# Kernel tuning notes

Measured on AMD Instinct MI355X. Metric: run time of the kernel, lower is better.

Reference implementation:

```python
import jax, jax.numpy as jnp
import numpy as np

B, N, E = 64, 512, 8192          # graphs, nodes per graph, edges per graph
F_IN, H, C = 128, 128, 10        # in features, hidden, classes
K1, K2 = 256, 128                # dense pool cluster counts: ceil(.5*N), ceil(.5*K1)
EPS = 1e-15


def setup_inputs():
    key = jax.random.key(0)
    keys = jax.random.split(key, 32)
    it = iter(keys)
    def w(shape, fan_in):
        return jax.random.normal(next(it), shape, jnp.float32) / np.sqrt(fan_in)
    x = jax.random.normal(next(it), (B * N, F_IN), jnp.float32)
    src_l = jax.random.randint(next(it), (B, E), 0, N)
    dst_l = jax.random.randint(next(it), (B, E), 0, N)
    off = (jnp.arange(B) * N)[:, None]
    src = (src_l + off).reshape(-1).astype(jnp.int32)
    dst = (dst_l + off).reshape(-1).astype(jnp.int32)
    return dict(
        x=x, src=src, dst=dst,
        conv0_wr=w((F_IN, H), F_IN), conv0_wroot=w((F_IN, H), F_IN), conv0_b=jnp.zeros((H,), jnp.float32),
        sconv2_wr=w((H, H), H), sconv2_wroot=w((H, H), H), sconv2_b=jnp.zeros((H,), jnp.float32),
        sconv3_wr=w((H, H), H), sconv3_wroot=w((H, H), H), sconv3_b=jnp.zeros((H,), jnp.float32),
        sage1_wr=w((H, H), H), sage1_wroot=w((H, H), H), sage1_b=jnp.zeros((H,), jnp.float32),
        sage2_wr=w((H, H), H), sage2_wroot=w((H, H), H), sage2_b=jnp.zeros((H,), jnp.float32),
        pool0_w=w((H, K1), H), pool0_b=jnp.zeros((K1,), jnp.float32),
        pool1_w=w((H, K2), H), pool1_b=jnp.zeros((K2,), jnp.float32),
        p1=w((H,), H), p2=w((H,), H), p3=w((H,), H),
        lin1_1_w=w((2 * H, H), 2 * H), lin1_1_b=jnp.zeros((H,), jnp.float32),
        lin1_w=w((H, H), H), lin1_b=jnp.zeros((H,), jnp.float32),
        lin2_w=w((2 * H, C), 2 * H), lin2_b=jnp.zeros((C,), jnp.float32),
    )


def _graph_conv(x, src, dst, emask, wr, wroot, b, n):
    # PyG GraphConv: lin_rel(sum_j x_j) + lin_root(x_i); invalid edges masked to 0.
    msg = x[src] * emask[:, None]
    agg = jax.ops.segment_sum(msg, dst, num_segments=n)
    return agg @ wr + x @ wroot + b


def _topk_pool(x, score_w, src, dst, emask, n_per_graph, k):
    # TopK pooling (MPoolS): score = x.w/||w||, keep top ratio*n per graph, gate by tanh(score).
    score = x @ score_w / (jnp.linalg.norm(score_w) + 1e-16)
    idx = jax.lax.top_k(score.reshape(B, n_per_graph), k)[1]
    perm = (idx + (jnp.arange(B) * n_per_graph)[:, None]).reshape(-1)
    new_x = x[perm] * jnp.tanh(score[perm])[:, None]
    new_id = jnp.full((B * n_per_graph,), -1, jnp.int32).at[perm].set(
        jnp.arange(B * k, dtype=jnp.int32))
    ns, nd = new_id[src], new_id[dst]
    valid = (ns >= 0) & (nd >= 0) & (emask > 0)
    return new_x, jnp.where(valid, ns, 0), jnp.where(valid, nd, 0), valid.astype(x.dtype)


def _readout(x, k):
    # gmp || gap per graph (nodes are contiguous, k per graph)
    xr = x.reshape(B, k, -1)
    return jnp.concatenate([xr.max(axis=1), xr.mean(axis=1)], axis=-1)


def _dense_sage(x, adj, wr, wroot, b):
    agg = (adj @ x) / jnp.clip(adj.sum(-1, keepdims=True), 1.0, None)
    return agg @ wr + x @ wroot + b


def _dense_mincut_pool(x, adj, s):
    s = jax.nn.softmax(s, axis=-1)
    k = s.shape[-1]
    out = jnp.einsum('bnk,bnf->bkf', s, x)
    out_adj = jnp.einsum('bnk,bnm,bml->bkl', s, adj, s)
    mincut_num = jnp.trace(out_adj, axis1=-2, axis2=-1)
    deg = adj.sum(-1)
    mincut_den = jnp.einsum('bn,bnk,bnk->b', deg, s, s)
    mc = -jnp.mean(mincut_num / (mincut_den + EPS))
    ss = jnp.einsum('bnk,bnl->bkl', s, s)
    ss_n = jnp.linalg.norm(ss, axis=(1, 2), keepdims=True)
    eye = jnp.eye(k, dtype=x.dtype)
    o = jnp.mean(jnp.linalg.norm(ss / (ss_n + EPS) - eye / jnp.sqrt(k), axis=(1, 2)))
    di = jnp.arange(k)
    out_adj = out_adj.at[:, di, di].set(0.0)
    dpool = jnp.sqrt(out_adj.sum(-1)) + EPS
    out_adj = out_adj / dpool[:, :, None] / dpool[:, None, :]
    return out, out_adj, mc, o


def _forward(x, src, dst, conv0_wr, conv0_wroot, conv0_b, sconv2_wr, sconv2_wroot, sconv2_b,
             sconv3_wr, sconv3_wroot, sconv3_b, sage1_wr, sage1_wroot, sage1_b,
             sage2_wr, sage2_wroot, sage2_b, pool0_w, pool0_b, pool1_w, pool1_b,
             p1, p2, p3, lin1_1_w, lin1_1_b, lin1_w, lin1_b, lin2_w, lin2_b):
    relu = jax.nn.relu
    e0 = jnp.ones((src.shape[0],), x.dtype)
    x0 = relu(_graph_conv(x, src, dst, e0, conv0_wr, conv0_wroot, conv0_b, B * N))
    # ---- sparse (MPoolS / top-k) branch, stage 1 ----
    sx, s1, d1, m1 = _topk_pool(x0, p1, src, dst, e0, N, N // 2)
    sx1 = _readout(sx, N // 2)
    # ---- dense (DiffPool-style) branch ----
    xd = x0.reshape(B, N, H)                               # to_dense_batch (full mask)
    g = src // N
    adj = jnp.zeros((B, N, N), x.dtype).at[g, src % N, dst % N].add(1.0)  # to_dense_adj
    s = xd @ pool0_w + pool0_b
    xd, adj, mc, o = _dense_mincut_pool(xd, adj, s)
    xd = relu(_dense_sage(xd, adj, sage1_wr, sage1_wroot, sage1_b))
    s = xd @ pool1_w + pool1_b
    xd, adj, mc2, o2 = _dense_mincut_pool(xd, adj, s)
    mc, o = mc + mc2, o + o2
    xd = _dense_sage(xd, adj, sage2_wr, sage2_wroot, sage2_b)
    xg = relu(xd.mean(axis=1) @ lin1_w + lin1_b)
    # ---- sparse branch, stages 2 and 3 ----
    sx = relu(_graph_conv(sx, s1, d1, m1, sconv2_wr, sconv2_wroot, sconv2_b, B * (N // 2)))
    sx, s2, d2, m2 = _topk_pool(sx, p2, s1, d1, m1, N // 2, N // 4)
    sx2 = _readout(sx, N // 4)
    sx = relu(_graph_conv(sx, s2, d2, m2, sconv3_wr, sconv3_wroot, sconv3_b, B * (N // 4)))
    sx, s3, d3, m3 = _topk_pool(sx, p3, s2, d2, m2, N // 4, N // 8)
    sx3 = _readout(sx, N // 8)
    sxr = relu((sx1 + sx2 + sx3) @ lin1_1_w + lin1_1_b)
    logits = jnp.concatenate([sxr, xg], axis=-1) @ lin2_w + lin2_b
    return logits, mc, o


def reference(x, src, dst, conv0_wr, conv0_wroot, conv0_b, sconv2_wr, sconv2_wroot, sconv2_b,
              sconv3_wr, sconv3_wroot, sconv3_b, sage1_wr, sage1_wroot, sage1_b,
              sage2_wr, sage2_wroot, sage2_b, pool0_w, pool0_b, pool1_w, pool1_b,
              p1, p2, p3, lin1_1_w, lin1_1_b, lin1_w, lin1_b, lin2_w, lin2_b):
    return _forward(x, src, dst, conv0_wr, conv0_wroot, conv0_b, sconv2_wr, sconv2_wroot,
                    sconv2_b, sconv3_wr, sconv3_wroot, sconv3_b, sage1_wr, sage1_wroot,
                    sage1_b, sage2_wr, sage2_wroot, sage2_b, pool0_w, pool0_b, pool1_w,
                    pool1_b, p1, p2, p3, lin1_1_w, lin1_1_b, lin1_w, lin1_b, lin2_w, lin2_b)
```

## Files before the change

kernel.cpp:

```cpp
#include <hip/hip_runtime.h>
#include <math.h>

#define NGRAPH 64
#define NE 524288
#define EPG 8192
#define TSZ 2560

typedef short s16x8 __attribute__((ext_vector_type(8)));
typedef float f32x4 __attribute__((ext_vector_type(4)));

__device__ inline unsigned short f2bf(float f) {
    unsigned int u = __float_as_uint(f);
    return (unsigned short)((u + 0x7FFFu + ((u >> 16) & 1u)) >> 16);
}

__global__ void edge_count2(const int* __restrict__ keyA, int* __restrict__ cntA,
                            const int* __restrict__ keyB, int* __restrict__ cntB) {
    int e = blockIdx.x * 256 + threadIdx.x;
    if (e >= NE) return;
    if (blockIdx.y == 0) atomicAdd(&cntA[keyA[e]], 1);
    else                 atomicAdd(&cntB[keyB[e]], 1);
}

__device__ inline void scan_body(const int* __restrict__ counts, int* __restrict__ offs,
                                 int* __restrict__ cursor, int nPerGraph,
                                 float* __restrict__ degOut, int* s) {
    const int g = blockIdx.x, t = threadIdx.x;
    int v = (t < nPerGraph) ? counts[g * nPerGraph + t] : 0;
    s[t] = v; __syncthreads();
    for (int d = 1; d < 512; d <<= 1) {
        int u = (t >= d) ? s[t - d] : 0;
        __syncthreads();
        s[t] += u;
        __syncthreads();
    }
    if (t < nPerGraph) {
        int o = g * EPG + s[t] - v;
        offs[g * nPerGraph + t] = o;
        cursor[g * nPerGraph + t] = o;
        if (degOut) degOut[g * nPerGraph + t] = (float)v;
    }
}

__global__ __launch_bounds__(512) void scan_offsets(const int* __restrict__ counts,
        int* __restrict__ offs, int* __restrict__ cursor, int nPerGraph,
        float* __restrict__ degOut) {
    __shared__ int s[512];
    scan_body(counts, offs, cursor, nPerGraph, degOut, s);
}

__global__ __launch_bounds__(512) void scan_offsets2(
        const int* __restrict__ cA, int* __restrict__ oA, int* __restrict__ uA,
        const int* __restrict__ cB, int* __restrict__ oB, int* __restrict__ uB,
        int nPerGraph, float* __restrict__ degB) {
    __shared__ int s[512];
    if (blockIdx.y == 0) scan_body(cA, oA, uA, nPerGraph, nullptr, s);
    else                 scan_body(cB, oB, uB, nPerGraph, degB, s);
}

__global__ void edge_fill(const int* __restrict__ key, const int* __restrict__ payload,
                          const float* __restrict__ mask, int* __restrict__ cursor,
                          int* __restrict__ elist) {
    int e = blockIdx.x * 256 + threadIdx.x;
    if (e < NE && (!mask || mask[e] > 0.f)) {
        int p = atomicAdd(&cursor[key[e]], 1);
        elist[p] = payload[e];
    }
}

__global__ void edge_fill2(const int* __restrict__ kA, const int* __restrict__ pA,
                           int* __restrict__ uA, int* __restrict__ eA,
                           const int* __restrict__ kB, const int* __restrict__ pB,
                           int* __restrict__ uB, int* __restrict__ eB) {
    int e = blockIdx.x * 256 + threadIdx.x;
    if (e >= NE) return;
    if (blockIdx.y == 0) { int p = atomicAdd(&uA[kA[e]], 1); eA[p] = pA[e]; }
    else                 { int p = atomicAdd(&uB[kB[e]], 1); eB[p] = pB[e]; }
}

__global__ __launch_bounds__(256) void gather_csr(
    const float* __restrict__ xfeat, int Fx,
    const int* __restrict__ offs, const int* __restrict__ cnts,
    const int* __restrict__ elist,
    float* __restrict__ out, int totRows, int rowsPerGraph)
{
    const int gid = (blockIdx.x * 256 + threadIdx.x) >> 5;
    const int lane = threadIdx.x & 31;
    const int csh = (Fx == 256) ? 1 : 0;
    const int rid = gid >> csh;
    const int c0 = (gid & ((1 << csh) - 1)) << 7;
    if (rid >= totRows) return;
    const int row = (rid & 63) * rowsPerGraph + (rid >> 6);
    const int beg = offs[row];
    const int n = cnts[row];
    const long long co = (long long)c0 + (lane << 2);
    float4 acc = make_float4(0.f, 0.f, 0.f, 0.f);
    int j = 0;
    for (; j + 4 <= n; j += 4) {
        const int n0 = elist[beg + j], n1 = elist[beg + j + 1];
        const int n2 = elist[beg + j + 2], n3 = elist[beg + j + 3];
        const float4 v0 = *(const float4*)&xfeat[(long long)n0 * Fx + co];
        const float4 v1 = *(const float4*)&xfeat[(long long)n1 * Fx + co];
        const float4 v2 = *(const float4*)&xfeat[(long long)n2 * Fx + co];
        const float4 v3 = *(const float4*)&xfeat[(long long)n3 * Fx + co];
        acc.x += v0.x + v1.x + v2.x + v3.x;
        acc.y += v0.y + v1.y + v2.y + v3.y;
        acc.z += v0.z + v1.z + v2.z + v3.z;
        acc.w += v0.w + v1.w + v2.w + v3.w;
    }
    for (; j < n; ++j) {
        const float4 v = *(const float4*)&xfeat[(long long)elist[beg + j] * Fx + co];
        acc.x += v.x; acc.y += v.y; acc.z += v.z; acc.w += v.w;
    }
    *(float4*)&out[(long long)row * Fx + co] = acc;
}

struct WSpec {
    const float* w1; const float* w2; int K1; int K2; int Nn;
    unsigned short* oh; unsigned short* ol;
};

__global__ void wconv_all(WSpec s0, WSpec s1, WSpec s2, WSpec s3, WSpec s4, WSpec s5, WSpec s6) {
    WSpec s;
    switch (blockIdx.y) {
        case 0: s = s0; break; case 1: s = s1; break; case 2: s = s2; break;
        case 3: s = s3; break; case 4: s = s4; break; case 5: s = s5; break;
        default: s = s6; break;
    }
    int idx = blockIdx.x * 256 + threadIdx.x;
    int Kt = s.K1 + s.K2;
    if (idx >= s.Nn * Kt) return;
    int n = idx / Kt, k = idx - n * Kt;
    float v = (k < s.K1) ? s.w1[(long long)k * s.Nn + n] : s.w2[(long long)(k - s.K1) * s.Nn + n];
    unsigned short h = f2bf(v);
    s.oh[idx] = h;
    s.ol[idx] = f2bf(v - __uint_as_float((unsigned int)h << 16));
}

__device__ inline void stageN_split(const float* __restrict__ src, int ldk, int k0,
                                    short* lds, int tid, const float* __restrict__ rs, int m0) {
    const int r = tid >> 2, kq = (tid & 3) << 3;
    const float* p = src + (long long)r * ldk + k0 + kq;
    float v[8];
    *(float4*)v = *(const float4*)p;
    *(float4*)(v + 4) = *(const float4*)(p + 4);
    if (rs) { float s = rs[m0 + r]; for (int i = 0; i < 8; ++i) v[i] *= s; }
    s16x8 hv, lv;
    #pragma unroll
    for (int i = 0; i < 8; ++i) {
        unsigned short h = f2bf(v[i]);
        float hf = __uint_as_float((unsigned int)h << 16);
        hv[i] = (short)h;
        lv[i] = (short)f2bf(v[i] - hf);
    }
    *(s16x8*)(lds + r * 40 + kq) = hv;
    *(s16x8*)(lds + TSZ + r * 40 + kq) = lv;
}

__device__ inline void stageT_split(const float* __restrict__ src, int ldm, int k0, int m0,
                                    short* lds, int tid) {
    const int kp = tid >> 4, mc = tid & 15;
    const int k = kp << 1;
    const float* p0 = src + (long long)(k0 + k) * ldm + m0 + mc;
    const float* p1 = p0 + ldm;
    #pragma unroll
    for (int i = 0; i < 4; ++i) {
        float a = p0[i << 4], b = p1[i << 4];
        unsigned short ha = f2bf(a), hb = f2bf(b);
        float hfa = __uint_as_float((unsigned int)ha << 16);
        float hfb = __uint_as_float((unsigned int)hb << 16);
        unsigned short la = f2bf(a - hfa), lb = f2bf(b - hfb);
        const int o = (mc + (i << 4)) * 40 + k;
        *(unsigned int*)(lds + o) = (unsigned int)ha | ((unsigned int)hb << 16);
        *(unsigned int*)(lds + o + TSZ) = (unsigned int)la | ((unsigned int)lb << 16);
    }
}

__device__ inline void stageT_hi(const float* __restrict__ src, int ldm, int k0, int m0,
                                 short* lds, int tid) {
    const int kp = tid >> 4, mc = tid & 15;
    const int k = kp << 1;
    const float* p0 = src + (long long)(k0 + k) * ldm + m0 + mc;
    const float* p1 = p0 + ldm;
    #pragma unroll
    for (int i = 0; i < 4; ++i) {
        unsigned short ha = f2bf(p0[i << 4]), hb = f2bf(p1[i << 4]);
        *(unsigned int*)(lds + (mc + (i << 4)) * 40 + k) =
            (unsigned int)ha | ((unsigned int)hb << 16);
    }
}

__device__ inline void stageW_split(const unsigned short* __restrict__ wh,
                                    const unsigned short* __restrict__ wl, int ldk,
                                    int n0, int k0, short* lds, int tid) {
    const int r = tid >> 2, kq = (tid & 3) << 3;
    *(s16x8*)(lds + r * 40 + kq) = *(const s16x8*)(wh + (long long)(n0 + r) * ldk + k0 + kq);
    *(s16x8*)(lds + TSZ + r * 40 + kq) = *(const s16x8*)(wl + (long long)(n0 + r) * ldk + k0 + kq);
}

__device__ inline void mfma_split(const short* As, const short* Bs, int wm, int wn,
                                  int l15, int quad, f32x4 (&acc)[2][2]) {
    const int ko = quad << 3;
    s16x8 ah[2], al[2], bh[2], bl[2];
    #pragma unroll
    for (int i = 0; i < 2; ++i) {
        const int ra = (wm + (i << 4) + l15) * 40 + ko;
        const int rb = (wn + (i << 4) + l15) * 40 + ko;
        ah[i] = *(const s16x8*)&As[ra];
        al[i] = *(const s16x8*)&As[TSZ + ra];
        bh[i] = *(const s16x8*)&Bs[rb];
        bl[i] = *(const s16x8*)&Bs[TSZ + rb];
    }
    #pragma unroll
    for (int mi = 0; mi < 2; ++mi)
    #pragma unroll
    for (int ni = 0; ni < 2; ++ni) {
        f32x4 c = acc[mi][ni];
        c = __builtin_amdgcn_mfma_f32_16x16x32_bf16(ah[mi], bh[ni], c, 0, 0, 0);
        c = __builtin_amdgcn_mfma_f32_16x16x32_bf16(ah[mi], bl[ni], c, 0, 0, 0);
        c = __builtin_amdgcn_mfma_f32_16x16x32_bf16(al[mi], bh[ni], c, 0, 0, 0);
        acc[mi][ni] = c;
    }
}

__device__ inline void mfma_hi(const short* As, const short* Bs, int wm, int wn,
                               int l15, int quad, f32x4 (&acc)[2][2]) {
    const int ko = quad << 3;
    s16x8 ah[2], bh[2];
    #pragma unroll
    for (int i = 0; i < 2; ++i) {
        ah[i] = *(const s16x8*)&As[(wm + (i << 4) + l15) * 40 + ko];
        bh[i] = *(const s16x8*)&Bs[(wn + (i << 4) + l15) * 40 + ko];
    }
    #pragma unroll
    for (int mi = 0; mi < 2; ++mi)
    #pragma unroll
    for (int ni = 0; ni < 2; ++ni)
        acc[mi][ni] = __builtin_amdgcn_mfma_f32_16x16x32_bf16(ah[mi], bh[ni], acc[mi][ni], 0, 0, 0);
}

__global__ __launch_bounds__(256) void gemm_aw(
    const float* __restrict__ A1, int K1, const float* __restrict__ A2, int K2,
    const float* __restrict__ rscale,
    const unsigned short* __restrict__ Wh, const unsigned short* __restrict__ Wl,
    const float* __restrict__ bias, float* __restrict__ C, int Nn, int doRelu)
{
    __shared__ short As[2 * TSZ], Bs[2 * TSZ];
    const int m0 = blockIdx.y << 6, n0 = blockIdx.x << 6;
    const int tid = threadIdx.x, lane = tid & 63, wv = tid >> 6;
    const int l15 = lane & 15, quad = lane >> 4;
    const int wm = (wv & 1) << 5, wn = (wv >> 1) << 5;
    f32x4 acc[2][2] = {};
    const int Kt = K1 + K2;
    for (int k0 = 0; k0 < Kt; k0 += 32) {
        if (k0 < K1) stageN_split(A1 + (long long)m0 * K1, K1, k0, As, tid, rscale, m0);
        else         stageN_split(A2 + (long long)m0 * K2, K2, k0 - K1, As, tid, nullptr, 0);
        stageW_split(Wh, Wl, Kt, n0, k0, Bs, tid);
        __syncthreads();
        mfma_split(As, Bs, wm, wn, l15, quad, acc);
        __syncthreads();
    }
    #pragma unroll
    for (int mi = 0; mi < 2; ++mi)
    #pragma unroll
    for (int ni = 0; ni < 2; ++ni) {
        const int col = n0 + wn + (ni << 4) + l15;
        const float bv = bias ? bias[col] : 0.f;
        #pragma unroll
        for (int r = 0; r < 4; ++r) {
            const int row = m0 + wm + (mi << 4) + (quad << 2) + r;
            float v = acc[mi][ni][r] + bv;
            if (doRelu) v = fmaxf(v, 0.f);
            C[(long long)row * Nn + col] = v;
        }
    }
}

__global__ __launch_bounds__(256) void gemm_tt(
    const float* __restrict__ At, const float* __restrict__ Bkn,
    float* __restrict__ C, float* __restrict__ fro,
    int Kd, int Mm, int Nn, int dual,
    long long sA, long long sB, long long sC)
{
    __shared__ short As[2 * TSZ], Bs[2 * TSZ], A2s[TSZ];
    __shared__ float redf[4];
    const int z = blockIdx.x;
    const float* Ap = At + (long long)z * sA;
    const float* Bp = Bkn + (long long)z * sB;
    const int m0 = blockIdx.y << 6, n0 = blockIdx.z << 6;
    const int tid = threadIdx.x, lane = tid & 63, wv = tid >> 6;
    const int l15 = lane & 15, quad = lane >> 4;
    const int wm = (wv & 1) << 5, wn = (wv >> 1) << 5;
    const int fw = dual ? ((m0 < n0) ? 2 : ((m0 == n0) ? 1 : 0)) : 0;
    f32x4 acc[2][2] = {};
    f32x4 accA[2][2] = {};
    for (int k0 = 0; k0 < Kd; k0 += 32) {
        stageT_split(Ap, Mm, k0, m0, As, tid);
        stageT_split(Bp, Nn, k0, n0, Bs, tid);
        if (fw) stageT_hi(Ap, Mm, k0, n0, A2s, tid);
        __syncthreads();
        mfma_split(As, Bs, wm, wn, l15, quad, acc);
        if (fw) mfma_hi(As, A2s, wm, wn, l15, quad, accA);
        __syncthreads();
    }
    float* Cp = C + (long long)z * sC;
    #pragma unroll
    for (int mi = 0; mi < 2; ++mi)
    #pragma unroll
    for (int ni = 0; ni < 2; ++ni) {
        const int col = n0 + wn + (ni << 4) + l15;
        #pragma unroll
        for (int r = 0; r < 4; ++r) {
            const int row = m0 + wm + (mi << 4) + (quad << 2) + r;
            Cp[(long long)row * Nn + col] = acc[mi][ni][r];
        }
    }
    if (fw) {
        float s = 0.f;
        #pragma unroll
        for (int mi = 0; mi < 2; ++mi)
        #pragma unroll
        for (int ni = 0; ni < 2; ++ni)
        #pragma unroll
        for (int r = 0; r < 4; ++r) s += accA[mi][ni][r] * accA[mi][ni][r];
        s *= (float)fw;
        for (int off = 32; off; off >>= 1) s += __shfl_xor(s, off);
        if (lane == 0) redf[wv] = s;
        __syncthreads();
        if (tid == 0) atomicAdd(&fro[z], redf[0] + redf[1] + redf[2] + redf[3]);
    }
}

__global__ __launch_bounds__(256) void gemm_nt(
    const float* __restrict__ A, const float* __restrict__ Bkn, float* __restrict__ C,
    int Kd, int Nn, long long sA, long long sB, long long sC)
{
    __shared__ short As[2 * TSZ], Bs[2 * TSZ];
    const int z = blockIdx.x;
    const int m0 = blockIdx.y << 6, n0 = blockIdx.z << 6;
    const float* Ap = A + (long long)z * sA + (long long)m0 * Kd;
    const float* Bp = Bkn + (long long)z * sB;
    const int tid = threadIdx.x, lane = tid & 63, wv = tid >> 6;
    const int l15 = lane & 15, quad = lane >> 4;
    const int wm = (wv & 1) << 5, wn = (wv >> 1) << 5;
    f32x4 acc[2][2] = {};
    for (int k0 = 0; k0 < Kd; k0 += 32) {
        stageN_split(Ap, Kd, k0, As, tid, nullptr, 0);
        stageT_split(Bp, Nn, k0, n0, Bs, tid);
        __syncthreads();
        mfma_split(As, Bs, wm, wn, l15, quad, acc);
        __syncthreads();
    }
    float* Cp = C + (long long)z * sC;
    #pragma unroll
    for (int mi = 0; mi < 2; ++mi)
    #pragma unroll
    for (int ni = 0; ni < 2; ++ni) {
        const int col = n0 + wn + (ni << 4) + l15;
        #pragma unroll
        for (int r = 0; r < 4; ++r) {
            const int row = m0 + wm + (mi << 4) + (quad << 2) + r;
            Cp[(long long)row * Nn + col] = acc[mi][ni][r];
        }
    }
}

__global__ __launch_bounds__(256) void softmax_rows_wave(
    float* __restrict__ sm, int L,
    const float* __restrict__ deg,
    float* __restrict__ rowq2, float* __restrict__ rowdq2, int totRows)
{
    const int wid = (blockIdx.x * 256 + threadIdx.x) >> 6;
    const int lane = threadIdx.x & 63;
    if (wid >= totRows) return;
    float* rowp = sm + (long long)wid * L;
    const int nv = L >> 6;
    float v[4];
    if (nv == 4) {
        float4 t = *(const float4*)&rowp[lane << 2];
        v[0] = t.x; v[1] = t.y; v[2] = t.z; v[3] = t.w;
    } else {
        float2 t = *(const float2*)&rowp[lane << 1];
        v[0] = t.x; v[1] = t.y;
    }
    float mx = v[0];
    for (int i = 1; i < nv; ++i) mx = fmaxf(mx, v[i]);
    for (int off = 32; off; off >>= 1) mx = fmaxf(mx, __shfl_xor(mx, off));
    float s = 0.f;
    for (int i = 0; i < nv; ++i) { v[i] = expf(v[i] - mx); s += v[i]; }
    for (int off = 32; off; off >>= 1) s += __shfl_xor(s, off);
    const float inv = 1.f / s;
    float q2 = 0.f;
    for (int i = 0; i < nv; ++i) { float p = v[i] * inv; v[i] = p; q2 += p * p; }
    if (nv == 4) *(float4*)&rowp[lane << 2] = make_float4(v[0], v[1], v[2], v[3]);
    else         *(float2*)&rowp[lane << 1] = make_float2(v[0], v[1]);
    for (int off = 32; off; off >>= 1) q2 += __shfl_xor(q2, off);
    if (lane == 0) { rowq2[wid] = q2; rowdq2[wid] = deg[wid] * q2; }
}

__global__ __launch_bounds__(256) void zdiag_rowsum_wave(
    float* __restrict__ adj, int K, float* __restrict__ dpool,
    float* __restrict__ rowdiag, int totRows)
{
    const int wid = (blockIdx.x * 256 + threadIdx.x) >> 6;
    const int lane = threadIdx.x & 63;
    if (wid >= totRows) return;
    const int b = wid / K;
    const int dcol = wid - b * K;
    float* rowp = adj + (long long)wid * K;
    const int nv = K >> 6;
    float s = 0.f, dval = 0.f;
    for (int q = 0; q < nv; ++q) {
        int c = lane + (q << 6);
        float v = rowp[c];
        if (c == dcol) { dval = v; rowp[c] = 0.f; v = 0.f; }
        s += v;
    }
    for (int off = 32; off; off >>= 1) s += __shfl_xor(s, off);
    if (lane == (dcol & 63)) rowdiag[wid] = dval;
    if (lane == 0) dpool[wid] = sqrtf(s) + 1e-15f;
}

__global__ __launch_bounds__(256) void norm_adj_wave(
    float* __restrict__ adj, int K, const float* __restrict__ dpool,
    float* __restrict__ rowsum, float* __restrict__ rscale, int totRows)
{
    const int wid = (blockIdx.x * 256 + threadIdx.x) >> 6;
    const int lane = threadIdx.x & 63;
    if (wid >= totRows) return;
    const int b = wid / K;
    float* rowp = adj + (long long)wid * K;
    const float inv_r = 1.f / dpool[wid];
    const int nv = K >> 6;
    float s = 0.f;
    for (int q = 0; q < nv; ++q) {
        int c = lane + (q << 6);
        float v = rowp[c] * inv_r / dpool[b * K + c];
        rowp[c] = v;
        s += v;
    }
    for (int off = 32; off; off >>= 1) s += __shfl_xor(s, off);
    if (lane == 0) { rowsum[wid] = s; rscale[wid] = 1.f / fmaxf(s, 1.f); }
}

__global__ __launch_bounds__(256) void reduce2_pergraph(
    const float* __restrict__ a, const float* __restrict__ b, int rowsPerGraph,
    float* __restrict__ outA, float* __restrict__ outB)
{
    __shared__ float redA[4], redB[4];
    const int g = blockIdx.x, t = threadIdx.x;
    float sa = 0.f, sb = 0.f;
    for (int i = t; i < rowsPerGraph; i += 256) {
        sa += a[g * rowsPerGraph + i];
        if (b) sb += b[g * rowsPerGraph + i];
    }
    for (int off = 32; off; off >>= 1) { sa += __shfl_xor(sa, off); sb += __shfl_xor(sb, off); }
    const int wv = t >> 6;
    if ((t & 63) == 0) { redA[wv] = sa; redB[wv] = sb; }
    __syncthreads();
    if (t == 0) {
        outA[g] = redA[0] + redA[1] + redA[2] + redA[3];
        if (outB) outB[g] = redB[0] + redB[1] + redB[2] + redB[3];
    }
}

__global__ __launch_bounds__(512) void topk_kernel(
    const float* __restrict__ x, const float* __restrict__ p, int n, int k,
    int* __restrict__ new_id, int* __restrict__ sel, float* __restrict__ gate)
{
    __shared__ float sc[512];
    __shared__ int pref[512];
    const int g = blockIdx.x, tid = threadIdx.x;
    float myScore = 0.f;
    if (tid < n) {
        const float* xr = x + (long long)(g * n + tid) * 128;
        float pn2 = 0.f, d = 0.f;
        #pragma unroll 4
        for (int f = 0; f < 128; f += 4) {
            float4 pv = *(const float4*)&p[f];
            float4 v = *(const float4*)&xr[f];
            pn2 += pv.x * pv.x + pv.y * pv.y + pv.z * pv.z + pv.w * pv.w;
            d += v.x * pv.x + v.y * pv.y + v.z * pv.z + v.w * pv.w;
        }
        myScore = d / (sqrtf(pn2) + 1e-16f);
        sc[tid] = myScore;
    }
    __syncthreads();
    int keep = 0;
    if (tid < n) {
        const float si = myScore;
        int rank = 0;
        for (int j = 0; j < n; j += 4) {
// ... 167 lines not shown
    char* w = (char*)d_ws;
    const unsigned long long MBy = 1ull << 20;
    float* x0    = (float*)(w + 0);
    float* BIG1  = (float*)(w + 16 * MBy);
    float* BIG2  = (float*)(w + 48 * MBy);
    float* agg   = (float*)(w + 80 * MBy);
    float* outx1 = (float*)(w + 96 * MBy);
    float* adj1  = (float*)(w + 104 * MBy);
    int*   s1    = (int*)(w + 120 * MBy);
    int*   d1    = (int*)(w + 122 * MBy);
    float* m1    = (float*)(w + 124 * MBy);
    int*   s2e   = (int*)(w + 126 * MBy);
    int*   d2e   = (int*)(w + 128 * MBy);
    float* m2e   = (float*)(w + 130 * MBy);
    char*  misc  = w + 132 * MBy;
    float* score = (float*)(misc);
    int*   sel   = (int*)(misc + 128 * 1024);
    float* gate  = (float*)(misc + 192 * 1024);
    int*   newid = (int*)(misc + 256 * 1024);
    float* deg   = (float*)(misc + 384 * 1024);
    float* dpool = (float*)(misc + 512 * 1024);
    float* rowsum2 = (float*)(misc + 576 * 1024);
    float* rscale2 = (float*)(misc + 640 * 1024);
    float* dpool2  = (float*)(misc + 704 * 1024);
    float* rowsum3 = (float*)(misc + 736 * 1024);
    float* rscale3 = (float*)(misc + 768 * 1024);
    float* accs    = (float*)(misc + 800 * 1024);
    float* sxsum   = (float*)(misc + 900 * 1024);
    float* xg      = (float*)(misc + 964 * 1024);

    unsigned short* wt_sg1h   = (unsigned short*)(misc + 1024 * 1024);
    unsigned short* wt_sg1l   = wt_sg1h + 32768;
    unsigned short* wt_sg2h   = wt_sg1l + 32768;
    unsigned short* wt_sg2l   = wt_sg2h + 32768;
    unsigned short* wt_pool0h = wt_sg2l + 32768;
    unsigned short* wt_pool0l = wt_pool0h + 32768;
    unsigned short* wt_pool1h = wt_pool0l + 32768;
    unsigned short* wt_pool1l = wt_pool1h + 32768;
    unsigned short* wt_c0h    = wt_pool1l + 32768;
    unsigned short* wt_c0l    = wt_c0h + 32768;
    unsigned short* wt_sc2h   = wt_c0l + 32768;
    unsigned short* wt_sc2l   = wt_sc2h + 32768;
    unsigned short* wt_sc3h   = wt_sc2l + 32768;
    unsigned short* wt_sc3l   = wt_sc3h + 32768;

    float* pmax = (float*)(misc + 2048 * 1024);
    float* psum = pmax + 32768;

    float* rowq2  = score;
    float* rowdq2 = (float*)newid;
    float* rowdiag = (float*)sel;

    float* s_sm  = BIG1;
    float* Tbuf  = BIG2;
    float* xd1   = BIG2;
    float* AX    = BIG2 + 2 * 1024 * 1024;
    float* s2sm  = BIG2 + 4 * 1024 * 1024;
    float* T2    = BIG2 + 6 * 1024 * 1024;
    float* outx2 = BIG1;
    float* adj2b = BIG1 + 1024 * 1024;
    float* xd2   = BIG1 + 2 * 1024 * 1024;
    float* sxA   = BIG1 + 3 * 1024 * 1024;
    float* sxE   = BIG1 + 5 * 1024 * 1024;
    float* sxB   = x0;
    float* sxC   = x0 + 2 * 1024 * 1024;
    float* sxD   = x0 + 3 * 1024 * 1024;

    char* adjc = (char*)adj1;
    int* elA  = (int*)(adjc + 0);
    int* elB  = (int*)(adjc + 2 * MBy);
    int* cntA = (int*)(adjc + 4 * MBy);
    int* cntB = (int*)(adjc + 4 * MBy + 128 * 1024);
    int* offA = (int*)(adjc + 4 * MBy + 256 * 1024);
    int* curA = (int*)(adjc + 4 * MBy + 384 * 1024);
    int* offB = (int*)(adjc + 4 * MBy + 512 * 1024);
    int* curB = (int*)(adjc + 4 * MBy + 640 * 1024);
    char* aggc = (char*)agg;
    int* elC  = (int*)(aggc + 8 * MBy);
    int* elD  = (int*)(aggc + 10 * MBy);
    int* cntC = (int*)(aggc + 12 * MBy);
    int* offC = (int*)(aggc + 12 * MBy + 256 * 1024);
    int* curC = (int*)(aggc + 12 * MBy + 512 * 1024);
    int* cntD = (int*)(aggc + 13 * MBy);
    int* offD = (int*)(aggc + 13 * MBy + 256 * 1024);
    int* curD = (int*)(aggc + 13 * MBy + 512 * 1024);

    hipMemsetAsync(accs, 0, 520 * sizeof(float), stream);
    hipMemsetAsync(sxsum, 0, 16384 * sizeof(float), stream);
    hipMemsetAsync(cntA, 0, 65536 * sizeof(int), stream);

    {
        WSpec a{sg1_wr, sg1_wrt, 128, 128, 128, wt_sg1h, wt_sg1l};
        WSpec b{sg2_wr, sg2_wrt, 128, 128, 128, wt_sg2h, wt_sg2l};
        WSpec c{pool0_w, nullptr, 128, 0, 256, wt_pool0h, wt_pool0l};
        WSpec d{pool1_w, nullptr, 128, 0, 128, wt_pool1h, wt_pool1l};
        WSpec e{conv0_wr, conv0_wrt, 128, 128, 128, wt_c0h, wt_c0l};
        WSpec f{sc2_wr, sc2_wrt, 128, 128, 128, wt_sc2h, wt_sc2l};
        WSpec g{sc3_wr, sc3_wrt, 128, 128, 128, wt_sc3h, wt_sc3l};
        wconv_all<<<dim3(128, 7), 256, 0, stream>>>(a, b, c, d, e, f, g);
    }

    edge_count2<<<dim3(2048, 2), 256, 0, stream>>>(dst, cntA, src, cntB);
    scan_offsets2<<<dim3(64, 2), 512, 0, stream>>>(cntA, offA, curA, cntB, offB, curB, 512, deg);
    edge_fill2<<<dim3(2048, 2), 256, 0, stream>>>(dst, src, curA, elA, src, dst, curB, elB);

    gather_csr<<<4096, 256, 0, stream>>>(x, 128, offA, cntA, elA, agg, 32768, 512);
    gemm_aw<<<dim3(2, 512), 256, 0, stream>>>(agg, 128, x, 128, nullptr, wt_c0h, wt_c0l,
        conv0_b, x0, 128, 1);

    gemm_aw<<<dim3(4, 512), 256, 0, stream>>>(x0, 128, nullptr, 0, nullptr, wt_pool0h, wt_pool0l,
        pool0_b, s_sm, 256, 0);
    softmax_rows_wave<<<8192, 256, 0, stream>>>(s_sm, 256, deg, rowq2, rowdq2, 32768);
    reduce2_pergraph<<<64, 256, 0, stream>>>(rowq2, rowdq2, 512, accs + 128, accs + 64);
    gather_csr<<<8192, 256, 0, stream>>>(s_sm, 256, offB, cntB, elB, Tbuf, 32768, 512);
    gemm_tt<<<dim3(64, 4, 2), 256, 0, stream>>>(s_sm, x0, outx1, nullptr, 512, 256, 128, 0,
        512 * 256, 512 * 128, 256 * 128);
    gemm_tt<<<dim3(64, 4, 4), 256, 0, stream>>>(s_sm, Tbuf, adj1, accs + 192, 512, 256, 256, 1,
        512 * 256, 512 * 256, 256 * 256);
    zdiag_rowsum_wave<<<4096, 256, 0, stream>>>(adj1, 256, dpool, rowdiag, 16384);
    reduce2_pergraph<<<64, 256, 0, stream>>>(rowdiag, nullptr, 256, accs + 0, nullptr);
    norm_adj_wave<<<4096, 256, 0, stream>>>(adj1, 256, dpool, rowsum2, rscale2, 16384);
    gemm_nt<<<dim3(64, 4, 2), 256, 0, stream>>>(adj1, outx1, AX, 256, 128,
        256 * 256, 256 * 128, 256 * 128);
    gemm_aw<<<dim3(2, 256), 256, 0, stream>>>(AX, 128, outx1, 128, rscale2, wt_sg1h, wt_sg1l,
        sg1_b, xd1, 128, 1);
    gemm_aw<<<dim3(2, 256), 256, 0, stream>>>(xd1, 128, nullptr, 0, nullptr, wt_pool1h, wt_pool1l,
        pool1_b, s2sm, 128, 0);
    softmax_rows_wave<<<4096, 256, 0, stream>>>(s2sm, 128, rowsum2, rowq2, rowdq2, 16384);
    reduce2_pergraph<<<64, 256, 0, stream>>>(rowq2, rowdq2, 256, accs + 384, accs + 320);
    gemm_nt<<<dim3(64, 4, 2), 256, 0, stream>>>(adj1, s2sm, T2, 256, 128,
        256 * 256, 256 * 128, 256 * 128);
    gemm_tt<<<dim3(64, 2, 2), 256, 0, stream>>>(s2sm, xd1, outx2, nullptr, 256, 128, 128, 0,
        256 * 128, 256 * 128, 128 * 128);
    gemm_tt<<<dim3(64, 2, 2), 256, 0, stream>>>(s2sm, T2, adj2b, accs + 448, 256, 128, 128, 1,
        256 * 128, 256 * 128, 128 * 128);
    zdiag_rowsum_wave<<<2048, 256, 0, stream>>>(adj2b, 128, dpool2, rowdiag, 8192);
    reduce2_pergraph<<<64, 256, 0, stream>>>(rowdiag, nullptr, 128, accs + 256, nullptr);
    norm_adj_wave<<<2048, 256, 0, stream>>>(adj2b, 128, dpool2, rowsum3, rscale3, 8192);
    gemm_nt<<<dim3(64, 2, 2), 256, 0, stream>>>(adj2b, outx2, AX, 128, 128,
        128 * 128, 128 * 128, 128 * 128);
    gemm_aw<<<dim3(2, 128), 256, 0, stream>>>(AX, 128, outx2, 128, rscale3, wt_sg2h, wt_sg2l,
        sg2_b, xd2, 128, 0);
    mean_lin<<<64, 128, 0, stream>>>(xd2, l1_w, l1_b, xg, 128);

    topk_kernel<<<64, 512, 0, stream>>>(x0, p1, 512, 256, newid, sel, gate);
    gather_gate<<<2048, 256, 0, stream>>>(x0, sel, gate, sxA, 16384);
    hipMemsetAsync(cntC, 0, 16384 * sizeof(int), stream);
    remap_edges_count<<<2048, 256, 0, stream>>>(src, dst, nullptr, newid, s1, d1, m1, cntC);
    readout_part<<<dim3(64, 4), 128, 0, stream>>>(sxA, 256, pmax, psum);
    readout_comb<<<64, 128, 0, stream>>>(pmax, psum, 256, sxsum);
    scan_offsets<<<64, 512, 0, stream>>>(cntC, offC, curC, 256, nullptr);
    edge_fill<<<2048, 256, 0, stream>>>(d1, s1, m1, curC, elC);
    gather_csr<<<2048, 256, 0, stream>>>(sxA, 128, offC, cntC, elC, agg, 16384, 256);
    gemm_aw<<<dim3(2, 256), 256, 0, stream>>>(agg, 128, sxA, 128, nullptr, wt_sc2h, wt_sc2l,
        sc2_b, sxB, 128, 1);
    topk_kernel<<<64, 512, 0, stream>>>(sxB, p2, 256, 128, newid, sel, gate);
    gather_gate<<<1024, 256, 0, stream>>>(sxB, sel, gate, sxC, 8192);
    hipMemsetAsync(cntD, 0, 8192 * sizeof(int), stream);
    remap_edges_count<<<2048, 256, 0, stream>>>(s1, d1, m1, newid, s2e, d2e, m2e, cntD);
    readout_part<<<dim3(64, 4), 128, 0, stream>>>(sxC, 128, pmax, psum);
    readout_comb<<<64, 128, 0, stream>>>(pmax, psum, 128, sxsum);
    scan_offsets<<<64, 512, 0, stream>>>(cntD, offD, curD, 128, nullptr);
    edge_fill<<<2048, 256, 0, stream>>>(d2e, s2e, m2e, curD, elD);
    gather_csr<<<1024, 256, 0, stream>>>(sxC, 128, offD, cntD, elD, agg, 8192, 128);
    gemm_aw<<<dim3(2, 128), 256, 0, stream>>>(agg, 128, sxC, 128, nullptr, wt_sc3h, wt_sc3l,
        sc3_b, sxD, 128, 1);
    topk_kernel<<<64, 512, 0, stream>>>(sxD, p3, 128, 64, newid, sel, gate);
    gather_gate<<<512, 256, 0, stream>>>(sxD, sel, gate, sxE, 4096);
    readout_part<<<dim3(64, 4), 128, 0, stream>>>(sxE, 64, pmax, psum);
    readout_comb<<<64, 128, 0, stream>>>(pmax, psum, 64, sxsum);

    final_head<<<64, 128, 0, stream>>>(sxsum, l11_w, l11_b, xg, l2_w, l2_b, accs, out);
}
```

Baseline: 655.7 us.

## Precompute bf16 hi/lo splits in producer epilogues instead of GEMM staging

Producer kernels (gather, gemm_aw, gemm_tt, gemm_nt, softmax, norm_adj) now also write hi/lo bf16 split copies of their outputs. The batched GEMMs then load these pre-split halves directly, so they no longer convert fp32 to bf16 pairs in every tile stage, which was repeated across many blocks. In exchange the producers do extra stores and use more workspace, and norm_adj no longer writes the normalized fp32 adjacency back in place.

```diff
diff --git a/kernel.cpp b/kernel.cpp
--- a/kernel.cpp
+++ b/kernel.cpp
@@ -12,6 +12,9 @@
 __device__ inline unsigned short f2bf(float f) {
     unsigned int u = __float_as_uint(f);
     return (unsigned short)((u + 0x7FFFu + ((u >> 16) & 1u)) >> 16);
+}
+__device__ inline float bf2f(unsigned short h) {
+    return __uint_as_float((unsigned int)h << 16);
 }
 
 __global__ void edge_count2(const int* __restrict__ keyA, int* __restrict__ cntA,
@@ -82,7 +85,8 @@
     const float* __restrict__ xfeat, int Fx,
     const int* __restrict__ offs, const int* __restrict__ cnts,
     const int* __restrict__ elist,
-    float* __restrict__ out, int totRows, int rowsPerGraph)
+    float* __restrict__ out, unsigned short* __restrict__ oh, unsigned short* __restrict__ ol,
+    int totRows, int rowsPerGraph)
 {
     const int gid = (blockIdx.x * 256 + threadIdx.x) >> 5;
     const int lane = threadIdx.x & 31;
@@ -112,7 +116,18 @@
         const float4 v = *(const float4*)&xfeat[(long long)elist[beg + j] * Fx + co];
         acc.x += v.x; acc.y += v.y; acc.z += v.z; acc.w += v.w;
     }
-    *(float4*)&out[(long long)row * Fx + co] = acc;
+    if (oh) {
+        unsigned short h0 = f2bf(acc.x), h1 = f2bf(acc.y), h2 = f2bf(acc.z), h3 = f2bf(acc.w);
+        uint2 hv, lv;
+        hv.x = (unsigned int)h0 | ((unsigned int)h1 << 16);
+        hv.y = (unsigned int)h2 | ((unsigned int)h3 << 16);
+        lv.x = (unsigned int)f2bf(acc.x - bf2f(h0)) | ((unsigned int)f2bf(acc.y - bf2f(h1)) << 16);
+        lv.y = (unsigned int)f2bf(acc.z - bf2f(h2)) | ((unsigned int)f2bf(acc.w - bf2f(h3)) << 16);
+        *(uint2*)&oh[(long long)row * Fx + co] = hv;
+        *(uint2*)&ol[(long long)row * Fx + co] = lv;
+    } else {
+        *(float4*)&out[(long long)row * Fx + co] = acc;
+    }
 }
 
 struct WSpec {
@@ -157,36 +172,35 @@
     *(s16x8*)(lds + TSZ + r * 40 + kq) = lv;
 }
 
-__device__ inline void stageT_split(const float* __restrict__ src, int ldm, int k0, int m0,
-                                    short* lds, int tid) {
+__device__ inline void stageT_pre(const unsigned short* __restrict__ H,
+                                  const unsigned short* __restrict__ L,
+                                  int ldm, int k0, int m0, short* lds, int tid) {
     const int kp = tid >> 4, mc = tid & 15;
     const int k = kp << 1;
-    const float* p0 = src + (long long)(k0 + k) * ldm + m0 + mc;
-    const float* p1 = p0 + ldm;
+    const unsigned short* h0 = H + (long long)(k0 + k) * ldm + m0 + mc;
+    const unsigned short* h1 = h0 + ldm;
+    const unsigned short* l0 = L + (long long)(k0 + k) * ldm + m0 + mc;
+    const unsigned short* l1 = l0 + ldm;
     #pragma unroll
     for (int i = 0; i < 4; ++i) {
-        float a = p0[i << 4], b = p1[i << 4];
-        unsigned short ha = f2bf(a), hb = f2bf(b);
-        float hfa = __uint_as_float((unsigned int)ha << 16);
-        float hfb = __uint_as_float((unsigned int)hb << 16);
-        unsigned short la = f2bf(a - hfa), lb = f2bf(b - hfb);
         const int o = (mc + (i << 4)) * 40 + k;
-        *(unsigned int*)(lds + o) = (unsigned int)ha | ((unsigned int)hb << 16);
-        *(unsigned int*)(lds + o + TSZ) = (unsigned int)la | ((unsigned int)lb << 16);
-    }
-}
-
-__device__ inline void stageT_hi(const float* __restrict__ src, int ldm, int k0, int m0,
-                                 short* lds, int tid) {
+        *(unsigned int*)(lds + o) =
+            (unsigned int)h0[i << 4] | ((unsigned int)h1[i << 4] << 16);
+        *(unsigned int*)(lds + o + TSZ) =
+            (unsigned int)l0[i << 4] | ((unsigned int)l1[i << 4] << 16);
+    }
+}
+
+__device__ inline void stageT_hi_pre(const unsigned short* __restrict__ H,
+                                     int ldm, int k0, int m0, short* lds, int tid) {
     const int kp = tid >> 4, mc = tid & 15;
     const int k = kp << 1;
-    const float* p0 = src + (long long)(k0 + k) * ldm + m0 + mc;
-    const float* p1 = p0 + ldm;
+    const unsigned short* h0 = H + (long long)(k0 + k) * ldm + m0 + mc;
+    const unsigned short* h1 = h0 + ldm;
     #pragma unroll
     for (int i = 0; i < 4; ++i) {
-        unsigned short ha = f2bf(p0[i << 4]), hb = f2bf(p1[i << 4]);
         *(unsigned int*)(lds + (mc + (i << 4)) * 40 + k) =
-            (unsigned int)ha | ((unsigned int)hb << 16);
+            (unsigned int)h0[i << 4] | ((unsigned int)h1[i << 4] << 16);
     }
 }
 
@@ -243,7 +257,9 @@
     const float* __restrict__ A1, int K1, const float* __restrict__ A2, int K2,
     const float* __restrict__ rscale,
     const unsigned short* __restrict__ Wh, const unsigned short* __restrict__ Wl,
-    const float* __restrict__ bias, float* __restrict__ C, int Nn, int doRelu)
+    const float* __restrict__ bias, float* __restrict__ C,
+    unsigned short* __restrict__ Ch, unsigned short* __restrict__ Cl,
+    int Nn, int doRelu)
 {
     __shared__ short As[2 * TSZ], Bs[2 * TSZ];
     const int m0 = blockIdx.y << 6, n0 = blockIdx.x << 6;
@@ -272,21 +288,30 @@
             float v = acc[mi][ni][r] + bv;
             if (doRelu) v = fmaxf(v, 0.f);
             C[(long long)row * Nn + col] = v;
+            if (Ch) {
+                unsigned short h = f2bf(v);
+                Ch[(long long)row * Nn + col] = h;
+                Cl[(long long)row * Nn + col] = f2bf(v - bf2f(h));
+            }
         }
     }
 }
 
 __global__ __launch_bounds__(256) void gemm_tt(
-    const float* __restrict__ At, const float* __restrict__ Bkn,
-    float* __restrict__ C, float* __restrict__ fro,
+    const unsigned short* __restrict__ Ah, const unsigned short* __restrict__ Al,
+    const unsigned short* __restrict__ Bh, const unsigned short* __restrict__ Bl,
+    float* __restrict__ C, unsigned short* __restrict__ Ch, unsigned short* __restrict__ Cl,
+    float* __restrict__ fro,
     int Kd, int Mm, int Nn, int dual,
     long long sA, long long sB, long long sC)
 {
     __shared__ short As[2 * TSZ], Bs[2 * TSZ], A2s[TSZ];
     __shared__ float redf[4];
     const int z = blockIdx.x;
-    const float* Ap = At + (long long)z * sA;
-    const float* Bp = Bkn + (long long)z * sB;
+    const unsigned short* Aph = Ah + (long long)z * sA;
+    const unsigned short* Apl = Al + (long long)z * sA;
+    const unsigned short* Bph = Bh + (long long)z * sB;
+    const unsigned short* Bpl = Bl + (long long)z * sB;
     const int m0 = blockIdx.y << 6, n0 = blockIdx.z << 6;
     const int tid = threadIdx.x, lane = tid & 63, wv = tid >> 6;
     const int l15 = lane & 15, quad = lane >> 4;
@@ -295,15 +320,17 @@
     f32x4 acc[2][2] = {};
     f32x4 accA[2][2] = {};
     for (int k0 = 0; k0 < Kd; k0 += 32) {
-        stageT_split(Ap, Mm, k0, m0, As, tid);
-        stageT_split(Bp, Nn, k0, n0, Bs, tid);
-        if (fw) stageT_hi(Ap, Mm, k0, n0, A2s, tid);
+        stageT_pre(Aph, Apl, Mm, k0, m0, As, tid);
+        stageT_pre(Bph, Bpl, Nn, k0, n0, Bs, tid);
+        if (fw) stageT_hi_pre(Aph, Mm, k0, n0, A2s, tid);
         __syncthreads();
         mfma_split(As, Bs, wm, wn, l15, quad, acc);
         if (fw) mfma_hi(As, A2s, wm, wn, l15, quad, accA);
         __syncthreads();
     }
     float* Cp = C + (long long)z * sC;
+    unsigned short* Chp = Ch ? Ch + (long long)z * sC : nullptr;
+    unsigned short* Clp = Ch ? Cl + (long long)z * sC : nullptr;
     #pragma unroll
     for (int mi = 0; mi < 2; ++mi)
     #pragma unroll
@@ -312,7 +339,13 @@
         #pragma unroll
         for (int r = 0; r < 4; ++r) {
             const int row = m0 + wm + (mi << 4) + (quad << 2) + r;
-            Cp[(long long)row * Nn + col] = acc[mi][ni][r];
+            const float v = acc[mi][ni][r];
+            Cp[(long long)row * Nn + col] = v;
+            if (Chp) {
+                unsigned short h = f2bf(v);
+                Chp[(long long)row * Nn + col] = h;
+                Clp[(long long)row * Nn + col] = f2bf(v - bf2f(h));
+            }
         }
     }
     if (fw) {
@@ -332,26 +365,29 @@
 }
 
 __global__ __launch_bounds__(256) void gemm_nt(
-    const float* __restrict__ A, const float* __restrict__ Bkn, float* __restrict__ C,
+    const unsigned short* __restrict__ Ah, const unsigned short* __restrict__ Al,
+    const unsigned short* __restrict__ Bh, const unsigned short* __restrict__ Bl,
+    float* __restrict__ C, unsigned short* __restrict__ Ch, unsigned short* __restrict__ Cl,
     int Kd, int Nn, long long sA, long long sB, long long sC)
 {
     __shared__ short As[2 * TSZ], Bs[2 * TSZ];
     const int z = blockIdx.x;
     const int m0 = blockIdx.y << 6, n0 = blockIdx.z << 6;
-    const float* Ap = A + (long long)z * sA + (long long)m0 * Kd;
-    const float* Bp = Bkn + (long long)z * sB;
+    const unsigned short* Aph = Ah + (long long)z * sA;
+    const unsigned short* Apl = Al + (long long)z * sA;
+    const unsigned short* Bph = Bh + (long long)z * sB;
+    const unsigned short* Bpl = Bl + (long long)z * sB;
     const int tid = threadIdx.x, lane = tid & 63, wv = tid >> 6;
     const int l15 = lane & 15, quad = lane >> 4;
     const int wm = (wv & 1) << 5, wn = (wv >> 1) << 5;
     f32x4 acc[2][2] = {};
     for (int k0 = 0; k0 < Kd; k0 += 32) {
-        stageN_split(Ap, Kd, k0, As, tid, nullptr, 0);
-        stageT_split(Bp, Nn, k0, n0, Bs, tid);
+        stageW_split(Aph, Apl, Kd, m0, k0, As, tid);
+        stageT_pre(Bph, Bpl, Nn, k0, n0, Bs, tid);
         __syncthreads();
         mfma_split(As, Bs, wm, wn, l15, quad, acc);
         __syncthreads();
     }
-    float* Cp = C + (long long)z * sC;
     #pragma unroll
     for (int mi = 0; mi < 2; ++mi)
     #pragma unroll
@@ -360,7 +396,13 @@
         #pragma unroll
         for (int r = 0; r < 4; ++r) {
             const int row = m0 + wm + (mi << 4) + (quad << 2) + r;
-            Cp[(long long)row * Nn + col] = acc[mi][ni][r];
+            const float v = acc[mi][ni][r];
+            if (C) C[(long long)z * sC + (long long)row * Nn + col] = v;
+            if (Ch) {
+                unsigned short h = f2bf(v);
+                Ch[(long long)z * sC + (long long)row * Nn + col] = h;
+                Cl[(long long)z * sC + (long long)row * Nn + col] = f2bf(v - bf2f(h));
+            }
         }
     }
 }
@@ -368,7 +410,8 @@
 __global__ __launch_bounds__(256) void softmax_rows_wave(
     float* __restrict__ sm, int L,
     const float* __restrict__ deg,
-    float* __restrict__ rowq2, float* __restrict__ rowdq2, int totRows)
+    float* __restrict__ rowq2, float* __restrict__ rowdq2, int totRows,
+    unsigned short* __restrict__ oh, unsigned short* __restrict__ ol)
 {
     const int wid = (blockIdx.x * 256 + threadIdx.x) >> 6;
     const int lane = threadIdx.x & 63;
@@ -394,6 +437,21 @@
     for (int i = 0; i < nv; ++i) { float p = v[i] * inv; v[i] = p; q2 += p * p; }
     if (nv == 4) *(float4*)&rowp[lane << 2] = make_float4(v[0], v[1], v[2], v[3]);
     else         *(float2*)&rowp[lane << 1] = make_float2(v[0], v[1]);
+    unsigned short h[4], lo[4];
+    for (int i = 0; i < nv; ++i) { h[i] = f2bf(v[i]); lo[i] = f2bf(v[i] - bf2f(h[i])); }
+    const long long rb = (long long)wid * L;
+    if (nv == 4) {
+        uint2 hv, lv;
+        hv.x = (unsigned int)h[0] | ((unsigned int)h[1] << 16);
+        hv.y = (unsigned int)h[2] | ((unsigned int)h[3] << 16);
+        lv.x = (unsigned int)lo[0] | ((unsigned int)lo[1] << 16);
+        lv.y = (unsigned int)lo[2] | ((unsigned int)lo[3] << 16);
+        *(uint2*)&oh[rb + (lane << 2)] = hv;
+        *(uint2*)&ol[rb + (lane << 2)] = lv;
+    } else {
+        *(unsigned int*)&oh[rb + (lane << 1)] = (unsigned int)h[0] | ((unsigned int)h[1] << 16);
+        *(unsigned int*)&ol[rb + (lane << 1)] = (unsigned int)lo[0] | ((unsigned int)lo[1] << 16);
+    }
     for (int off = 32; off; off >>= 1) q2 += __shfl_xor(q2, off);
     if (lane == 0) { rowq2[wid] = q2; rowdq2[wid] = deg[wid] * q2; }
 }
@@ -422,22 +480,25 @@
 }
 
 __global__ __launch_bounds__(256) void norm_adj_wave(
-    float* __restrict__ adj, int K, const float* __restrict__ dpool,
-    float* __restrict__ rowsum, float* __restrict__ rscale, int totRows)
+    const float* __restrict__ adj, int K, const float* __restrict__ dpool,
+    float* __restrict__ rowsum, float* __restrict__ rscale,
+    unsigned short* __restrict__ oh, unsigned short* __restrict__ ol, int totRows)
 {
     const int wid = (blockIdx.x * 256 + threadIdx.x) >> 6;
     const int lane = threadIdx.x & 63;
     if (wid >= totRows) return;
     const int b = wid / K;
-    float* rowp = adj + (long long)wid * K;
+    const float* rowp = adj + (long long)wid * K;
     const float inv_r = 1.f / dpool[wid];
     const int nv = K >> 6;
     float s = 0.f;
     for (int q = 0; q < nv; ++q) {
         int c = lane + (q << 6);
         float v = rowp[c] * inv_r / dpool[b * K + c];
-        rowp[c] = v;
         s += v;
+        unsigned short h = f2bf(v);
+        oh[(long long)wid * K + c] = h;
+        ol[(long long)wid * K + c] = f2bf(v - bf2f(h));
     }
     for (int off = 32; off; off >>= 1) s += __shfl_xor(s, off);
     if (lane == 0) { rowsum[wid] = s; rscale[wid] = 1.f / fmaxf(s, 1.f); }
@@ -711,11 +772,13 @@
     float* rowdiag = (float*)sel;
 
     float* s_sm  = BIG1;
-    float* Tbuf  = BIG2;
+    unsigned short* Tbh = (unsigned short*)BIG2;
+    unsigned short* Tbl = (unsigned short*)((char*)BIG2 + 16 * MBy);
     float* xd1   = BIG2;
     float* AX    = BIG2 + 2 * 1024 * 1024;
     float* s2sm  = BIG2 + 4 * 1024 * 1024;
-    float* T2    = BIG2 + 6 * 1024 * 1024;
+    unsigned short* T2h = (unsigned short*)((char*)BIG2 + 24 * MBy);
+    unsigned short* T2l = (unsigned short*)((char*)BIG2 + 28 * MBy);
     float* outx2 = BIG1;
     float* adj2b = BIG1 + 1024 * 1024;
     float* xd2   = BIG1 + 2 * 1024 * 1024;
@@ -724,6 +787,23 @@
     float* sxB   = x0;
     float* sxC   = x0 + 2 * 1024 * 1024;
     float* sxD   = x0 + 3 * 1024 * 1024;
+
+    unsigned short* s_smh = (unsigned short*)(w + 136 * MBy);
+    unsigned short* s_sml = (unsigned short*)(w + 152 * MBy);
+    unsigned short* x0h   = (unsigned short*)(w + 168 * MBy);
+    unsigned short* x0l   = (unsigned short*)(w + 176 * MBy);
+    unsigned short* ox1h  = (unsigned short*)(w + 184 * MBy);
+    unsigned short* ox1l  = (unsigned short*)(w + 188 * MBy);
+    unsigned short* xd1h  = (unsigned short*)(w + 192 * MBy);
+    unsigned short* xd1l  = (unsigned short*)(w + 196 * MBy);
+    unsigned short* s2h   = (unsigned short*)(w + 200 * MBy);
+    unsigned short* s2l   = (unsigned short*)(w + 204 * MBy);
+    unsigned short* ox2h  = (unsigned short*)(w + 208 * MBy);
+    unsigned short* ox2l  = (unsigned short*)(w + 210 * MBy);
+    unsigned short* a1h   = (unsigned short*)(w + 212 * MBy);
+    unsigned short* a1l   = (unsigned short*)(w + 220 * MBy);
+    unsigned short* a2h   = (unsigned short*)(w + 228 * MBy);
+    unsigned short* a2l   = (unsigned short*)(w + 230 * MBy);
 
     char* adjc = (char*)adj1;
     int* elA  = (int*)(adjc + 0);
@@ -763,43 +843,43 @@
     scan_offsets2<<<dim3(64, 2), 512, 0, stream>>>(cntA, offA, curA, cntB, offB, curB, 512, deg);
     edge_fill2<<<dim3(2048, 2), 256, 0, stream>>>(dst, src, curA, elA, src, dst, curB, elB);
 
-    gather_csr<<<4096, 256, 0, stream>>>(x, 128, offA, cntA, elA, agg, 32768, 512);
+    gather_csr<<<4096, 256, 0, stream>>>(x, 128, offA, cntA, elA, agg, nullptr, nullptr, 32768, 512);
     gemm_aw<<<dim3(2, 512), 256, 0, stream>>>(agg, 128, x, 128, nullptr, wt_c0h, wt_c0l,
-        conv0_b, x0, 128, 1);
+        conv0_b, x0, x0h, x0l, 128, 1);
 
     gemm_aw<<<dim3(4, 512), 256, 0, stream>>>(x0, 128, nullptr, 0, nullptr, wt_pool0h, wt_pool0l,
-        pool0_b, s_sm, 256, 0);
-    softmax_rows_wave<<<8192, 256, 0, stream>>>(s_sm, 256, deg, rowq2, rowdq2, 32768);
+        pool0_b, s_sm, nullptr, nullptr, 256, 0);
+    softmax_rows_wave<<<8192, 256, 0, stream>>>(s_sm, 256, deg, rowq2, rowdq2, 32768, s_smh, s_sml);
     reduce2_pergraph<<<64, 256, 0, stream>>>(rowq2, rowdq2, 512, accs + 128, accs + 64);
-    gather_csr<<<8192, 256, 0, stream>>>(s_sm, 256, offB, cntB, elB, Tbuf, 32768, 512);
-    gemm_tt<<<dim3(64, 4, 2), 256, 0, stream>>>(s_sm, x0, outx1, nullptr, 512, 256, 128, 0,
-        512 * 256, 512 * 128, 256 * 128);
-    gemm_tt<<<dim3(64, 4, 4), 256, 0, stream>>>(s_sm, Tbuf, adj1, accs + 192, 512, 256, 256, 1,
-        512 * 256, 512 * 256, 256 * 256);
+    gather_csr<<<8192, 256, 0, stream>>>(s_sm, 256, offB, cntB, elB, nullptr, Tbh, Tbl, 32768, 512);
+    gemm_tt<<<dim3(64, 4, 2), 256, 0, stream>>>(s_smh, s_sml, x0h, x0l, outx1, ox1h, ox1l,
+        nullptr, 512, 256, 128, 0, 512 * 256, 512 * 128, 256 * 128);
+    gemm_tt<<<dim3(64, 4, 4), 256, 0, stream>>>(s_smh, s_sml, Tbh, Tbl, adj1, nullptr, nullptr,
+        accs + 192, 512, 256, 256, 1, 512 * 256, 512 * 256, 256 * 256);
     zdiag_rowsum_wave<<<4096, 256, 0, stream>>>(adj1, 256, dpool, rowdiag, 16384);
     reduce2_pergraph<<<64, 256, 0, stream>>>(rowdiag, nullptr, 256, accs + 0, nullptr);
-    norm_adj_wave<<<4096, 256, 0, stream>>>(adj1, 256, dpool, rowsum2, rscale2, 16384);
-    gemm_nt<<<dim3(64, 4, 2), 256, 0, stream>>>(adj1, outx1, AX, 256, 128,
-        256 * 256, 256 * 128, 256 * 128);
+    norm_adj_wave<<<4096, 256, 0, stream>>>(adj1, 256, dpool, rowsum2, rscale2, a1h, a1l, 16384);
+    gemm_nt<<<dim3(64, 4, 2), 256, 0, stream>>>(a1h, a1l, ox1h, ox1l, AX, nullptr, nullptr,
+        256, 128, 256 * 256, 256 * 128, 256 * 128);
     gemm_aw<<<dim3(2, 256), 256, 0, stream>>>(AX, 128, outx1, 128, rscale2, wt_sg1h, wt_sg1l,
-        sg1_b, xd1, 128, 1);
+        sg1_b, xd1, xd1h, xd1l, 128, 1);
     gemm_aw<<<dim3(2, 256), 256, 0, stream>>>(xd1, 128, nullptr, 0, nullptr, wt_pool1h, wt_pool1l,
-        pool1_b, s2sm, 128, 0);
-    softmax_rows_wave<<<4096, 256, 0, stream>>>(s2sm, 128, rowsum2, rowq2, rowdq2, 16384);
+        pool1_b, s2sm, nullptr, nullptr, 128, 0);
+    softmax_rows_wave<<<4096, 256, 0, stream>>>(s2sm, 128, rowsum2, rowq2, rowdq2, 16384, s2h, s2l);
     reduce2_pergraph<<<64, 256, 0, stream>>>(rowq2, rowdq2, 256, accs + 384, accs + 320);
-    gemm_nt<<<dim3(64, 4, 2), 256, 0, stream>>>(adj1, s2sm, T2, 256, 128,
-        256 * 256, 256 * 128, 256 * 128);
-    gemm_tt<<<dim3(64, 2, 2), 256, 0, stream>>>(s2sm, xd1, outx2, nullptr, 256, 128, 128, 0,
-        256 * 128, 256 * 128, 128 * 128);
-    gemm_tt<<<dim3(64, 2, 2), 256, 0, stream>>>(s2sm, T2, adj2b, accs + 448, 256, 128, 128, 1,
-        256 * 128, 256 * 128, 128 * 128);
+    gemm_nt<<<dim3(64, 4, 2), 256, 0, stream>>>(a1h, a1l, s2h, s2l, nullptr, T2h, T2l,
+        256, 128, 256 * 256, 256 * 128, 256 * 128);
+    gemm_tt<<<dim3(64, 2, 2), 256, 0, stream>>>(s2h, s2l, xd1h, xd1l, outx2, ox2h, ox2l,
+        nullptr, 256, 128, 128, 0, 256 * 128, 256 * 128, 128 * 128);
+    gemm_tt<<<dim3(64, 2, 2), 256, 0, stream>>>(s2h, s2l, T2h, T2l, adj2b, nullptr, nullptr,
+        accs + 448, 256, 128, 128, 1, 256 * 128, 256 * 128, 128 * 128);
     zdiag_rowsum_wave<<<2048, 256, 0, stream>>>(adj2b, 128, dpool2, rowdiag, 8192);
     reduce2_pergraph<<<64, 256, 0, stream>>>(rowdiag, nullptr, 128, accs + 256, nullptr);
-    norm_adj_wave<<<2048, 256, 0, stream>>>(adj2b, 128, dpool2, rowsum3, rscale3, 8192);
-    gemm_nt<<<dim3(64, 2, 2), 256, 0, stream>>>(adj2b, outx2, AX, 128, 128,
-        128 * 128, 128 * 128, 128 * 128);
+    norm_adj_wave<<<2048, 256, 0, stream>>>(adj2b, 128, dpool2, rowsum3, rscale3, a2h, a2l, 8192);
+    gemm_nt<<<dim3(64, 2, 2), 256, 0, stream>>>(a2h, a2l, ox2h, ox2l, AX, nullptr, nullptr,
+        128, 128, 128 * 128, 128 * 128, 128 * 128);
     gemm_aw<<<dim3(2, 128), 256, 0, stream>>>(AX, 128, outx2, 128, rscale3, wt_sg2h, wt_sg2l,
-        sg2_b, xd2, 128, 0);
+        sg2_b, xd2, nullptr, nullptr, 128, 0);
     mean_lin<<<64, 128, 0, stream>>>(xd2, l1_w, l1_b, xg, 128);
 
     topk_kernel<<<64, 512, 0, stream>>>(x0, p1, 512, 256, newid, sel, gate);
@@ -810,9 +890,9 @@
     readout_comb<<<64, 128, 0, stream>>>(pmax, psum, 256, sxsum);
     scan_offsets<<<64, 512, 0, stream>>>(cntC, offC, curC, 256, nullptr);
     edge_fill<<<2048, 256, 0, stream>>>(d1, s1, m1, curC, elC);
-    gather_csr<<<2048, 256, 0, stream>>>(sxA, 128, offC, cntC, elC, agg, 16384, 256);
+    gather_csr<<<2048, 256, 0, stream>>>(sxA, 128, offC, cntC, elC, agg, nullptr, nullptr, 16384, 256);
     gemm_aw<<<dim3(2, 256), 256, 0, stream>>>(agg, 128, sxA, 128, nullptr, wt_sc2h, wt_sc2l,
-        sc2_b, sxB, 128, 1);
+        sc2_b, sxB, nullptr, nullptr, 128, 1);
     topk_kernel<<<64, 512, 0, stream>>>(sxB, p2, 256, 128, newid, sel, gate);
     gather_gate<<<1024, 256, 0, stream>>>(sxB, sel, gate, sxC, 8192);
     hipMemsetAsync(cntD, 0, 8192 * sizeof(int), stream);
@@ -821,9 +901,9 @@
     readout_comb<<<64, 128, 0, stream>>>(pmax, psum, 128, sxsum);
     scan_offsets<<<64, 512, 0, stream>>>(cntD, offD, curD, 128, nullptr);
     edge_fill<<<2048, 256, 0, stream>>>(d2e, s2e, m2e, curD, elD);
-    gather_csr<<<1024, 256, 0, stream>>>(sxC, 128, offD, cntD, elD, agg, 8192, 128);
+    gather_csr<<<1024, 256, 0, stream>>>(sxC, 128, offD, cntD, elD, agg, nullptr, nullptr, 8192, 128);
     gemm_aw<<<dim3(2, 128), 256, 0, stream>>>(agg, 128, sxC, 128, nullptr, wt_sc3h, wt_sc3l,
-        sc3_b, sxD, 128, 1);
+        sc3_b, sxD, nullptr, nullptr, 128, 1);
     topk_kernel<<<64, 512, 0, stream>>>(sxD, p3, 128, 64, newid, sel, gate);
     gather_gate<<<512, 256, 0, stream>>>(sxD, sel, gate, sxE, 4096);
     readout_part<<<dim3(64, 4), 128, 0, stream>>>(sxE, 64, pmax, psum);
```

Result: slower. 722.9 us (+10.3%).
